# Kernel optimization log

Hardware: AMD Instinct MI355X
Metric: run time of the kernel (lower is better)

Reference implementation:

```python
import jax, jax.numpy as jnp
import numpy as np

GROUP = 8
BS = 4096
CH = 512


def setup_inputs() -> dict:
    key = jax.random.key(0)
    k1, k2 = jax.random.split(key)
    x = jax.random.normal(k1, (GROUP, BS, CH), dtype=jnp.float32)
    stdv = 1.0 / np.sqrt(CH)  # reset_parameters: uniform(-stdv, stdv), stdv = 1/sqrt(channels)
    weight = jax.random.uniform(k2, (GROUP, CH, CH), minval=-stdv, maxval=stdv, dtype=jnp.float32)
    return {"x": x, "weight": weight}


def reference(x, weight):
    """Sequential per-channel Householder reflections.

    x: (group, bs, channels); weight: (group, channels, channels).
    Step i uses v_i = weight[:, :, i] and applies
        x <- x - 2/(v^T v) * (x @ v) v^T
    """
    vs = jnp.transpose(weight, (2, 0, 1))  # (channels, group, channels): scan axis first

    def step(x, v):
        denom = jnp.sum(v * v, axis=-1)          # (group,)   v^T v
        proj = jnp.einsum('gbc,gc->gb', x, v)    # (group, bs) x @ v
        x = x - (2.0 / denom)[:, None, None] * proj[:, :, None] * v[:, None, :]
        return x, None

    x, _ = jax.lax.scan(step, x, vs)
    return x
```

## Files before the change

kernel.cpp:

```cpp
#include <hip/hip_runtime.h>

#define GROUP 8
#define BS 4096
#define CH 512
#define PW 32
#define NPANEL 16

typedef __attribute__((ext_vector_type(4))) float f32x4;
typedef __attribute__((ext_vector_type(8))) short bf16x8;
typedef __attribute__((ext_vector_type(8))) unsigned short u16x8;
typedef unsigned short u16;

static __device__ __forceinline__ u16 f2bf(float f) {
    unsigned int u = __builtin_bit_cast(unsigned int, f);
    u += 0x7FFFu + ((u >> 16) & 1u);
    return (u16)(u >> 16);
}
static __device__ __forceinline__ float bf2f(u16 h) {
    return __builtin_bit_cast(float, (unsigned int)h << 16);
}
static __device__ __forceinline__ void split8(const float* v, bf16x8& h, bf16x8& l) {
#pragma unroll
    for (int j = 0; j < 8; ++j) {
        u16 hu = f2bf(v[j]);
        h[j] = (short)hu;
        l[j] = (short)f2bf(v[j] - bf2f(hu));
    }
}
#define MFMA(a, b, c) __builtin_amdgcn_mfma_f32_16x16x32_bf16(a, b, c, 0, 0, 0)

typedef const __attribute__((address_space(1))) void* gas_t;
typedef __attribute__((address_space(3))) void* las_t;
static __device__ __forceinline__ void gload16(const void* g, void* l) {
    __builtin_amdgcn_global_load_lds((gas_t)g, (las_t)l, 16, 0, 0);
}


__global__ __launch_bounds__(1024) void k_panelprep(const float* __restrict__ w,
                                                    const float* __restrict__ x,
                                                    u16* __restrict__ Yfh,
                                                    u16* __restrict__ Yfl,
                                                    u16* __restrict__ Mfh,
                                                    u16* __restrict__ Mfl,
                                                    u16* __restrict__ Afh,
                                                    u16* __restrict__ Afl,
                                                    u16* __restrict__ xb) {
    __shared__ float Ylds[PW][516];
    __shared__ float Sp[16][PW][36];
    __shared__ float S_ls[PW][36];
    __shared__ float T_ls[PW][36];

    int bid = blockIdx.x;
    int t   = threadIdx.x;

    if (bid >= 128) {
        int bx  = bid - 128;
        int xcd = bx & 7;
        int j   = bx >> 3;
        const int UPG = (BS * CH) / 8;
        int base = xcd * UPG + j * (UPG / 128);
        for (int u = t; u < 2048; u += 1024) {
            int i = base + u;
            const float4* s = (const float4*)(x + (size_t)i * 8);
            float4 a = s[0], b = s[1];
            u16x8 o;
            o[0] = f2bf(a.x); o[1] = f2bf(a.y); o[2] = f2bf(a.z); o[3] = f2bf(a.w);
            o[4] = f2bf(b.x); o[5] = f2bf(b.y); o[6] = f2bf(b.z); o[7] = f2bf(b.w);
            *(u16x8*)(xb + (size_t)i * 8) = o;
        }
        return;
    }

    int pb   = (bid & 7) * 16 + (bid >> 3);
    int lane = t & 63;
    int wv   = t >> 6;
    int fr   = lane & 15;
    int kg   = lane >> 4;
    int g    = pb >> 4;
    int p    = pb & 15;
    int i0   = p * PW;

    const float* wg = w + (size_t)g * CH * CH;
    for (int idx4 = t; idx4 < 4096; idx4 += 1024) {
        int c = idx4 >> 3, f4 = idx4 & 7;
        float4 v = *(const float4*)(wg + (size_t)c * CH + i0 + f4 * 4);
        Ylds[f4 * 4 + 0][c] = v.x;
        Ylds[f4 * 4 + 1][c] = v.y;
        Ylds[f4 * 4 + 2][c] = v.z;
        Ylds[f4 * 4 + 3][c] = v.w;
    }
    __syncthreads();

    {
        f32x4 sacc[2][2];
#pragma unroll
        for (int a = 0; a < 2; ++a)
#pragma unroll
            for (int b = 0; b < 2; ++b)
#pragma unroll
                for (int z = 0; z < 4; ++z) sacc[a][b][z] = 0.f;
        {
            int kk = wv;
            bf16x8 fh[2], fl[2];
#pragma unroll
            for (int h = 0; h < 2; ++h) {
                float a8[8];
                const float* src = &Ylds[h * 16 + fr][kk * 32 + kg * 8];
#pragma unroll
                for (int j = 0; j < 8; ++j) a8[j] = src[j];
                split8(a8, fh[h], fl[h]);
            }
#pragma unroll
            for (int a = 0; a < 2; ++a)
#pragma unroll
                for (int b = 0; b < 2; ++b) {
                    sacc[a][b] = MFMA(fh[a], fh[b], sacc[a][b]);
                    sacc[a][b] = MFMA(fh[a], fl[b], sacc[a][b]);
                    sacc[a][b] = MFMA(fl[a], fh[b], sacc[a][b]);
                }
        }
#pragma unroll
        for (int a = 0; a < 2; ++a)
#pragma unroll
            for (int b = 0; b < 2; ++b)
#pragma unroll
                for (int j = 0; j < 4; ++j)
                    Sp[wv][a * 16 + kg * 4 + j][b * 16 + fr] = sacc[a][b][j];
    }
    __syncthreads();
    for (int idx = t; idx < PW * PW; idx += 1024) {
        int r = idx >> 5, c = idx & 31;
        float s = 0.f;
#pragma unroll
        for (int q = 0; q < 16; ++q) s += Sp[q][r][c];
        S_ls[r][c] = s;
    }
    __syncthreads();

    if (wv == 0) {
        float Trow[PW];
#pragma unroll
        for (int j = 0; j < PW; ++j) Trow[j] = 0.f;
        if (lane < PW) Trow[lane] = 2.0f / S_ls[lane][lane];
#pragma unroll
        for (int k = 1; k < PW; ++k) {
            float acc = 0.f;
#pragma unroll
            for (int j = 0; j < PW; ++j)
                if (j < k) acc += Trow[j] * S_ls[j][k];
            float bk = 2.0f / S_ls[k][k];
            if (lane < k) Trow[k] = -bk * acc;
        }
        if (lane < PW)
#pragma unroll
            for (int j = 0; j < PW; ++j) T_ls[lane][j] = Trow[j];
    }
    __syncthreads();

    u16* Msth = (u16*)Sp;
    u16* Mstl = Msth + 16384;
    {
        bf16x8 tbh[2], tbl[2];
#pragma unroll
        for (int cf = 0; cf < 2; ++cf) {
            float t8[8];
            const float* src = &T_ls[cf * 16 + fr][kg * 8];
#pragma unroll
            for (int j = 0; j < 8; ++j) t8[j] = src[j];
            split8(t8, tbh[cf], tbl[cf]);
        }
#pragma unroll
        for (int rfi = 0; rfi < 2; ++rfi) {
            int rf = 2 * wv + rfi;
            float a8[8];
#pragma unroll
            for (int j = 0; j < 8; ++j) a8[j] = Ylds[kg * 8 + j][rf * 16 + fr];
            bf16x8 ah, al;
            split8(a8, ah, al);
#pragma unroll
            for (int cf = 0; cf < 2; ++cf) {
                f32x4 m;
#pragma unroll
                for (int z = 0; z < 4; ++z) m[z] = 0.f;
                m = MFMA(ah, tbh[cf], m);
                m = MFMA(ah, tbl[cf], m);
                m = MFMA(al, tbh[cf], m);
#pragma unroll
                for (int j = 0; j < 4; ++j) {
                    int c  = rf * 16 + kg * 4 + j;
                    int ii = cf * 16 + fr;
                    int off = ((c >> 4)) * 512 + ((ii >> 3) * 16 + (c & 15)) * 8 + (ii & 7);
                    u16 hu = f2bf(m[j]);
                    Msth[off] = hu;
                    Mstl[off] = f2bf(m[j] - bf2f(hu));
                }
            }
        }
    }
    __syncthreads();
    {
        u16* Mfh_g = Mfh + (size_t)g * CH * CH + (size_t)p * 16384;
        u16* Mfl_g = Mfl + (size_t)g * CH * CH + (size_t)p * 16384;
        for (int idx = t; idx < 2048; idx += 1024) {
            *(bf16x8*)(Mfh_g + (size_t)idx * 8) = *(const bf16x8*)(Msth + idx * 8);
            *(bf16x8*)(Mfl_g + (size_t)idx * 8) = *(const bf16x8*)(Mstl + idx * 8);
        }
    }

    {
        u16* Yfh_g = Yfh + (size_t)g * CH * CH;
        u16* Yfl_g = Yfl + (size_t)g * CH * CH;
        for (int idx = t; idx < 32 * 64; idx += 1024) {
            int tile = idx >> 6, l2 = idx & 63;
            int itl = tile >> 4, ct = tile & 15;
            int row = l2 & 15, kgg = l2 >> 4;
            float a8[8];
            const float* src = &Ylds[itl * 16 + row][ct * 32 + kgg * 8];
#pragma unroll
            for (int j = 0; j < 8; ++j) a8[j] = src[j];
            bf16x8 h, l;
            split8(a8, h, l);
            size_t off = ((size_t)((2 * p + itl) * 16 + ct)) * 512 + (size_t)l2 * 8;
            *(bf16x8*)(Yfh_g + off) = h;
            *(bf16x8*)(Yfl_g + off) = l;
        }
    }

    {
        u16* Afh_g = Afh + (size_t)g * CH * CH;
        u16* Afl_g = Afl + (size_t)g * CH * CH;
        for (int idx = t; idx < 32 * 64; idx += 1024) {
            int mt = idx >> 6, l2 = idx & 63;
            int row = l2 & 15, kg2 = l2 >> 4;
            float a8[8];
#pragma unroll
            for (int j = 0; j < 8; ++j) a8[j] = Ylds[kg2 * 8 + j][mt * 16 + row];
            bf16x8 h, l;
            split8(a8, h, l);
            size_t off = ((size_t)(p * 32 + mt)) * 512 + (size_t)l2 * 8;
            *(bf16x8*)(Afh_g + off) = h;
            *(bf16x8*)(Afl_g + off) = l;
        }
    }
}

template<int W>
__global__ __launch_bounds__(512) void k_combine(const u16* __restrict__ Yfh,
                                                 const u16* __restrict__ Yfl,
                                                 u16* __restrict__ Mfh,
                                                 u16* __restrict__ Mfl) {
    constexpr int NF   = W / 16;
    constexpr int KSPL = (NF >= 8) ? 1 : 8 / NF;
    constexpr int CPW  = (NF + 7) / 8;

    __shared__ u16 MAh[16][520];
    __shared__ u16 MAl[16][520];
    __shared__ float Cl[16][W + 4];
    __shared__ float Cpart[(KSPL > 1) ? (KSPL - 1) : 1][16][W + 4];

    int bid = blockIdx.x;
    int cb  = (bid & 7) * 16 + (bid >> 3);
    int t = threadIdx.x, lane = t & 63, wv = t >> 6;
    int fr = lane & 15, kg = lane >> 4;
    int g  = cb >> 4;
    int sg = cb & 15;
    constexpr int SP = W / 16;
    int q  = sg / SP, rs = sg % SP;
    int i_top0 = 2 * q * W + rs * 16;
    int i_bot0 = 2 * q * W + W;

    const u16* Yfh_g = Yfh + (size_t)g * CH * CH;
    const u16* Yfl_g = Yfl + (size_t)g * CH * CH;
    u16* Mfh_g = Mfh + (size_t)g * CH * CH;
    u16* Mfl_g = Mfl + (size_t)g * CH * CH;

    int kt_top = i_top0 >> 5;
    int hh     = (i_top0 & 31) >> 3;

    for (int idx = t; idx < 1024; idx += 512) {
        int c = idx >> 1, sub = idx & 1;
        size_t off = ((size_t)(kt_top * 32 + (c >> 4))) * 512
                   + (size_t)((hh + sub) * 16 + (c & 15)) * 8;
        bf16x8 hv = *(const bf16x8*)(Mfh_g + off);
        bf16x8 lv = *(const bf16x8*)(Mfl_g + off);
#pragma unroll
        for (int j = 0; j < 8; ++j) {
            MAh[sub * 8 + j][c] = (u16)hv[j];
            MAl[sub * 8 + j][c] = (u16)lv[j];
        }
    }
    __syncthreads();

    int ibt = i_bot0 >> 4;

    if constexpr (KSPL == 1) {
        f32x4 accC[CPW];
#pragma unroll
        for (int nfi = 0; nfi < CPW; ++nfi)
#pragma unroll
            for (int z = 0; z < 4; ++z) accC[nfi][z] = 0.f;

        auto LOADY = [&](int ks, bf16x8* dh, bf16x8* dl) {
#pragma unroll
            for (int nfi = 0; nfi < CPW; ++nfi) {
                int nf = wv + 8 * nfi;
                size_t yo = ((size_t)((ibt + nf) * 16 + ks)) * 512 + (size_t)lane * 8;
                dh[nfi] = *(const bf16x8*)(Yfh_g + yo);
                dl[nfi] = *(const bf16x8*)(Yfl_g + yo);
            }
        };

        bf16x8 pbh[CPW], pbl[CPW];
        LOADY(0, pbh, pbl);
#pragma unroll
        for (int ks = 0; ks < 16; ++ks) {
            bf16x8 qbh[CPW], qbl[CPW];
            if (ks + 1 < 16) LOADY(ks + 1, qbh, qbl);
            bf16x8 ah = *(const bf16x8*)&MAh[fr][ks * 32 + kg * 8];
            bf16x8 al = *(const bf16x8*)&MAl[fr][ks * 32 + kg * 8];
#pragma unroll
            for (int nfi = 0; nfi < CPW; ++nfi) {
                accC[nfi] = MFMA(ah, pbh[nfi], accC[nfi]);
                accC[nfi] = MFMA(ah, pbl[nfi], accC[nfi]);
                accC[nfi] = MFMA(al, pbh[nfi], accC[nfi]);
            }
#pragma unroll
            for (int nfi = 0; nfi < CPW; ++nfi) { pbh[nfi] = qbh[nfi]; pbl[nfi] = qbl[nfi]; }
        }
#pragma unroll
        for (int nfi = 0; nfi < CPW; ++nfi) {
            int nf = wv + 8 * nfi;
#pragma unroll
            for (int jj = 0; jj < 4; ++jj)
                Cl[kg * 4 + jj][nf * 16 + fr] = accC[nfi][jj];
        }
        __syncthreads();
    } else {
        int nf  = wv % NF;
        int ksl = wv / NF;
        constexpr int KCH = 16 / KSPL;
        f32x4 accC;
#pragma unroll
        for (int z = 0; z < 4; ++z) accC[z] = 0.f;

        auto LOADY1 = [&](int ks, bf16x8& dh, bf16x8& dl) {
            size_t yo = ((size_t)((ibt + nf) * 16 + ks)) * 512 + (size_t)lane * 8;
            dh = *(const bf16x8*)(Yfh_g + yo);
            dl = *(const bf16x8*)(Yfl_g + yo);
        };

        bf16x8 pbh, pbl;
        LOADY1(ksl * KCH, pbh, pbl);
#pragma unroll
        for (int ki = 0; ki < KCH; ++ki) {
            int ks = ksl * KCH + ki;
            bf16x8 qbh, qbl;
            if (ki + 1 < KCH) LOADY1(ks + 1, qbh, qbl);
            bf16x8 ah = *(const bf16x8*)&MAh[fr][ks * 32 + kg * 8];
            bf16x8 al = *(const bf16x8*)&MAl[fr][ks * 32 + kg * 8];
            accC = MFMA(ah, pbh, accC);
            accC = MFMA(ah, pbl, accC);
            accC = MFMA(al, pbh, accC);
            pbh = qbh; pbl = qbl;
        }
        if (ksl == 0) {
#pragma unroll
            for (int jj = 0; jj < 4; ++jj)
                Cl[kg * 4 + jj][nf * 16 + fr] = accC[jj];
        } else {
#pragma unroll
            for (int jj = 0; jj < 4; ++jj)
                Cpart[ksl - 1][kg * 4 + jj][nf * 16 + fr] = accC[jj];
        }
        __syncthreads();
        for (int idx = t; idx < 16 * W; idx += 512) {
            int r = idx / W, c = idx - r * W;
            float s = Cl[r][c];
#pragma unroll
            for (int u = 0; u < KSPL - 1; ++u) s += Cpart[u][r][c];
            Cl[r][c] = s;
        }
        __syncthreads();
    }

    f32x4 accU[4];
#pragma unroll
    for (int ni = 0; ni < 4; ++ni)
#pragma unroll
        for (int z = 0; z < 4; ++z) accU[ni][z] = 0.f;

    int kt_bot = i_bot0 >> 5;
    constexpr int NKS2 = W / 32;

    auto LOADM = [&](int ks2, bf16x8* dh, bf16x8* dl) {
#pragma unroll
        for (int ni = 0; ni < 4; ++ni) {
            int ct = wv * 4 + ni;
            size_t mo = ((size_t)((kt_bot + ks2) * 32 + ct)) * 512 + (size_t)lane * 8;
            dh[ni] = *(const bf16x8*)(Mfh_g + mo);
            dl[ni] = *(const bf16x8*)(Mfl_g + mo);
        }
    };

    {
        bf16x8 mph[4], mpl[4];
        LOADM(0, mph, mpl);
#pragma unroll
        for (int ks2 = 0; ks2 < NKS2; ++ks2) {
            bf16x8 mqh[4], mql[4];
            if (ks2 + 1 < NKS2) LOADM(ks2 + 1, mqh, mql);
            float a8[8];
#pragma unroll
            for (int j = 0; j < 8; ++j) a8[j] = Cl[fr][ks2 * 32 + kg * 8 + j];
            bf16x8 ah2, al2;
            split8(a8, ah2, al2);
#pragma unroll
            for (int ni = 0; ni < 4; ++ni) {
                accU[ni] = MFMA(ah2, mph[ni], accU[ni]);
                accU[ni] = MFMA(ah2, mpl[ni], accU[ni]);
                accU[ni] = MFMA(al2, mph[ni], accU[ni]);
            }
#pragma unroll
            for (int ni = 0; ni < 4; ++ni) { mph[ni] = mqh[ni]; mpl[ni] = mql[ni]; }
        }
    }
#pragma unroll
    for (int ni = 0; ni < 4; ++ni) {
        int c = (wv * 4 + ni) * 16 + fr;
#pragma unroll
        for (int jj = 0; jj < 4; ++jj) {
            int il = kg * 4 + jj;
            float ma = bf2f(MAh[il][c]) + bf2f(MAl[il][c]);
            float m2 = ma - accU[ni][jj];
            u16 hu = f2bf(m2);
            MAh[il][c] = hu;
            MAl[il][c] = f2bf(m2 - bf2f(hu));
        }
    }
    __syncthreads();

    for (int idx = t; idx < 1024; idx += 512) {
        int c = idx >> 1, sub = idx & 1;
        bf16x8 hv, lv;
#pragma unroll
        for (int j = 0; j < 8; ++j) {
            hv[j] = (short)MAh[sub * 8 + j][c];
            lv[j] = (short)MAl[sub * 8 + j][c];
        }
        size_t off = ((size_t)(kt_top * 32 + (c >> 4))) * 512
                   + (size_t)((hh + sub) * 16 + (c & 15)) * 8;
        *(bf16x8*)(Mfh_g + off) = hv;
        *(bf16x8*)(Mfl_g + off) = lv;
    }
}

__global__ __launch_bounds__(256) void k_qbuild2(const u16* __restrict__ Afh,
                                                 const u16* __restrict__ Afl,
                                                 const u16* __restrict__ Mfh,
                                                 const u16* __restrict__ Mfl,
                                                 u16* __restrict__ Qt) {
    int bid = blockIdx.x;
    int qb  = (bid & 7) * 64 + (bid >> 3);
    int t = threadIdx.x, lane = t & 63, wv = t >> 6;
    int fr = lane & 15, kg = lane >> 4;
    int g  = qb >> 6;
    int tm = (qb >> 2) & 15, tn = qb & 3;
    int c0 = tm * 32;
    int d0 = tn * 128 + wv * 32;

    const u16* Afh_g = Afh + (size_t)g * CH * CH;
    const u16* Afl_g = Afl + (size_t)g * CH * CH;
    const u16* Mfh_g = Mfh + (size_t)g * CH * CH;
    const u16* Mfl_g = Mfl + (size_t)g * CH * CH;
    u16* Qt_g = Qt + (size_t)g * CH * CH;

    f32x4 acc[2][2];
#pragma unroll
    for (int mi = 0; mi < 2; ++mi)
#pragma unroll
        for (int ni = 0; ni < 2; ++ni)
#pragma unroll
            for (int z = 0; z < 4; ++z) acc[mi][ni][z] = 0.f;

    int mt0 = c0 >> 4;
    for (int ks = 0; ks < 16; ++ks) {
        bf16x8 ah[2], al[2], bh[2], bl[2];
#pragma unroll
        for (int mi = 0; mi < 2; ++mi) {
            size_t ao = ((size_t)(ks * 32 + mt0 + mi)) * 512 + (size_t)lane * 8;
            ah[mi] = *(const bf16x8*)(Afh_g + ao);
            al[mi] = *(const bf16x8*)(Afl_g + ao);
        }
#pragma unroll
        for (int ni = 0; ni < 2; ++ni) {
            int ct = (d0 >> 4) + ni;
            size_t mo = ((size_t)(ks * 32 + ct)) * 512 + (size_t)lane * 8;
            bh[ni] = *(const bf16x8*)(Mfh_g + mo);
            bl[ni] = *(const bf16x8*)(Mfl_g + mo);
        }
#pragma unroll
        for (int mi = 0; mi < 2; ++mi)
#pragma unroll
            for (int ni = 0; ni < 2; ++ni) {
                acc[mi][ni] = MFMA(ah[mi], bh[ni], acc[mi][ni]);
                acc[mi][ni] = MFMA(ah[mi], bl[ni], acc[mi][ni]);
                acc[mi][ni] = MFMA(al[mi], bh[ni], acc[mi][ni]);
            }
    }
#pragma unroll
    for (int mi = 0; mi < 2; ++mi)
#pragma unroll
        for (int ni = 0; ni < 2; ++ni) {
            int cb2 = c0 + mi * 16 + kg * 4;
            int d   = d0 + ni * 16 + fr;
            ushort4 h4;
            h4.x = f2bf(((cb2 + 0 == d) ? 1.0f : 0.0f) - acc[mi][ni][0]);
            h4.y = f2bf(((cb2 + 1 == d) ? 1.0f : 0.0f) - acc[mi][ni][1]);
            h4.z = f2bf(((cb2 + 2 == d) ? 1.0f : 0.0f) - acc[mi][ni][2]);
            h4.w = f2bf(((cb2 + 3 == d) ? 1.0f : 0.0f) - acc[mi][ni][3]);
            *(ushort4*)(Qt_g + (size_t)d * CH + cb2) = h4;
        }
}

__global__ __launch_bounds__(256) void k_gemm2(const u16* __restrict__ xb,
                                               const u16* __restrict__ Qt,
                                               float* __restrict__ out) {
    __shared__ u16 Ab[2][128 * 32];
    __shared__ u16 Bb[2][128 * 32];

    int bid0 = blockIdx.x;
    int wg = (bid0 & 7) * 128 + (bid0 >> 3);
    int g  = wg >> 7;
    int r  = wg & 127;
    int tm = r >> 2;
    int tn = r & 3;

    int t    = threadIdx.x;
    int lane = t & 63;
    int wv   = t >> 6;
    int wr   = wv >> 1, wc = wv & 1;
    int fr   = lane & 15, kg = lane >> 4;

    const u16* xg  = xb + (size_t)g * BS * CH + (size_t)tm * 128 * CH;
    const u16* Qtg = Qt + (size_t)g * CH * CH + (size_t)tn * 128 * CH;
    float* og = out + (size_t)g * BS * CH + (size_t)tm * 128 * CH + (size_t)tn * 128;

    f32x4 acc[4][4];
#pragma unroll
    for (int mi = 0; mi < 4; ++mi)
#pragma unroll
        for (int ni = 0; ni < 4; ++ni)
#pragma unroll
            for (int z = 0; z < 4; ++z) acc[mi][ni][z] = 0.f;

    int srow = lane >> 2;
    int scol = (lane & 3) * 8;

    auto STAGE = [&](int p, int ks) {
        int k0 = ks * 32;
#pragma unroll
        for (int si = 0; si < 2; ++si) {
            int seg = wv * 2 + si;
            int row = seg * 16 + srow;
            gload16(xg  + (size_t)row * CH + k0 + scol, &Ab[p][seg * 512]);
            gload16(Qtg + (size_t)row * CH + k0 + scol, &Bb[p][seg * 512]);
        }
    };

    STAGE(0, 0);
    asm volatile("s_waitcnt vmcnt(0)" ::: "memory");
    __builtin_amdgcn_s_barrier();

    for (int ks = 0; ks < 16; ++ks) {
        int cur = ks & 1;
        if (ks < 15) {
            STAGE(cur ^ 1, ks + 1);
            asm volatile("s_waitcnt vmcnt(4)" ::: "memory");
        } else {
            asm volatile("s_waitcnt vmcnt(0)" ::: "memory");
        }
        __builtin_amdgcn_s_barrier();

        bf16x8 af[4], bfr[4];
#pragma unroll
        for (int mi = 0; mi < 4; ++mi)
            af[mi] = *(const bf16x8*)&Ab[cur][(wr * 64 + mi * 16 + fr) * 32 + kg * 8];
#pragma unroll
        for (int ni = 0; ni < 4; ++ni)
            bfr[ni] = *(const bf16x8*)&Bb[cur][(wc * 64 + ni * 16 + fr) * 32 + kg * 8];
        __builtin_amdgcn_s_setprio(1);
#pragma unroll
        for (int mi = 0; mi < 4; ++mi)
#pragma unroll
            for (int ni = 0; ni < 4; ++ni)
                acc[mi][ni] = MFMA(af[mi], bfr[ni], acc[mi][ni]);
        __builtin_amdgcn_s_setprio(0);

        asm volatile("" ::: "memory");
        __builtin_amdgcn_s_barrier();
    }

    int rg = lane >> 4;
#pragma unroll
    for (int mi = 0; mi < 4; ++mi)
#pragma unroll
        for (int ni = 0; ni < 4; ++ni)
#pragma unroll
            for (int rj = 0; rj < 4; ++rj) {
                int grow = wr * 64 + mi * 16 + rg * 4 + rj;
                int gcol = wc * 64 + ni * 16 + fr;
                og[(size_t)grow * CH + gcol] = acc[mi][ni][rj];
            }
}

#define LDP 40
__global__ __launch_bounds__(256) void k_gemm_f32(const float* __restrict__ x,
                                                  const u16* __restrict__ Qt,
                                                  float* __restrict__ out) {
    __shared__ u16 Al[128 * LDP];
    __shared__ u16 Bl[128 * LDP];

    int bid = blockIdx.x;
    int g  = bid >> 7;
    int tn = (bid >> 5) & 3;
    int tm = bid & 31;

    int t    = threadIdx.x;
    int lane = t & 63;
    int w    = t >> 6;
    int wr   = w >> 1, wc = w & 1;

    const float* xg = x + (size_t)g * BS * CH + (size_t)tm * 128 * CH;
    const u16* Qtg = Qt + (size_t)g * CH * CH + (size_t)tn * 128 * CH;
    float* og = out + (size_t)g * BS * CH + (size_t)tm * 128 * CH + (size_t)tn * 128;

    f32x4 acc[4][4];
#pragma unroll
    for (int mi = 0; mi < 4; ++mi)
#pragma unroll
        for (int ni = 0; ni < 4; ++ni)
#pragma unroll
            for (int z = 0; z < 4; ++z) acc[mi][ni][z] = 0.f;

    int a_k4 = t & 7;
    int a_r  = t >> 3;
    int b_n  = t & 127;
    int b_kh = t >> 7;
    int fr = lane & 15, kg = lane >> 4;

    for (int ks = 0; ks < 16; ++ks) {
        int k0 = ks * 32;
        __syncthreads();
#pragma unroll
        for (int rr = 0; rr < 4; ++rr) {
            int r = a_r + 32 * rr;
            float4 v = *(const float4*)(xg + (size_t)r * CH + k0 + a_k4 * 4);
            ushort4 h;
            h.x = f2bf(v.x); h.y = f2bf(v.y); h.z = f2bf(v.z); h.w = f2bf(v.w);
            *(ushort4*)(&Al[r * LDP + a_k4 * 4]) = h;
        }
        {
            const u16* src = Qtg + (size_t)b_n * CH + k0 + b_kh * 16;
            u16x8 lo = *(const u16x8*)src;
            u16x8 hi = *(const u16x8*)(src + 8);
            *(u16x8*)(&Bl[b_n * LDP + b_kh * 16]) = lo;
            *(u16x8*)(&Bl[b_n * LDP + b_kh * 16 + 8]) = hi;
        }
        __syncthreads();
        bf16x8 af[4], bfr[4];
#pragma unroll
        for (int mi = 0; mi < 4; ++mi)
            af[mi] = *(const bf16x8*)(&Al[(wr * 64 + mi * 16 + fr) * LDP + kg * 8]);
#pragma unroll
        for (int ni = 0; ni < 4; ++ni)
            bfr[ni] = *(const bf16x8*)(&Bl[(wc * 64 + ni * 16 + fr) * LDP + kg * 8]);
#pragma unroll
        for (int mi = 0; mi < 4; ++mi)
#pragma unroll
            for (int ni = 0; ni < 4; ++ni)
                acc[mi][ni] = MFMA(af[mi], bfr[ni], acc[mi][ni]);
    }

    int rg = lane >> 4;
#pragma unroll
    for (int mi = 0; mi < 4; ++mi)
#pragma unroll
        for (int ni = 0; ni < 4; ++ni)
#pragma unroll
            for (int rj = 0; rj < 4; ++rj) {
                int grow = wr * 64 + mi * 16 + rg * 4 + rj;
                int gcol = wc * 64 + ni * 16 + fr;
                og[(size_t)grow * CH + gcol] = acc[mi][ni][rj];
            }
}

extern "C" void kernel_launch(void* const* d_in, const int* in_sizes, int n_in,
                              void* d_out, int out_size, void* d_ws, size_t ws_size,
                              hipStream_t stream) {
    const float* x = (const float*)d_in[0];
    const float* w = (const float*)d_in[1];
    float* out = (float*)d_out;

    char* ob = (char*)d_out;
    u16* Yfh = (u16*)ob;
    u16* Yfl = (u16*)(ob + (4u  << 20));
    u16* Mfh = (u16*)(ob + (8u  << 20));
    u16* Mfl = (u16*)(ob + (12u << 20));
    u16* Afh = (u16*)(ob + (16u << 20));
    u16* Afl = (u16*)(ob + (20u << 20));

    int fat = (ws_size >= ((32u << 20) + (4u << 20))) ? 1 : 0;
    u16* xbp = (u16*)d_ws;
    u16* Qt  = fat ? (u16*)((char*)d_ws + (32u << 20)) : (u16*)d_ws;

    k_panelprep<<<dim3(fat ? 1152 : 128), dim3(1024), 0, stream>>>(w, x, Yfh, Yfl, Mfh, Mfl, Afh, Afl, xbp);
    k_combine<32><<<dim3(128), dim3(512), 0, stream>>>(Yfh, Yfl, Mfh, Mfl);
    k_combine<64><<<dim3(128), dim3(512), 0, stream>>>(Yfh, Yfl, Mfh, Mfl);
    k_combine<128><<<dim3(128), dim3(512), 0, stream>>>(Yfh, Yfl, Mfh, Mfl);
    k_combine<256><<<dim3(128), dim3(512), 0, stream>>>(Yfh, Yfl, Mfh, Mfl);
    k_qbuild2<<<dim3(512), dim3(256), 0, stream>>>(Afh, Afl, Mfh, Mfl, Qt);
    if (fat)
        k_gemm2<<<dim3(1024), dim3(256), 0, stream>>>(xbp, Qt, out);
    else
        k_gemm_f32<<<dim3(1024), dim3(256), 0, stream>>>(x, Qt, out);
}
```

Measured before the change: 102.0 us.

## Spread x bf16 cast across combine and qbuild kernels to fill idle CUs

The fp32-to-bf16 cast of x used to run entirely as extra blocks of the panel-prep kernel. It is now split by group: three groups stay in panelprep, one group goes to each of the four combine launches, and one to qbuild2, each as extra blocks appended to that grid. The combine kernels launch only 128 blocks, so the extra cast blocks are meant to use otherwise idle CUs and hide the bandwidth-bound cast behind latency-bound stages. The cost is larger grids and more code in those kernels, and the cast blocks may compete for bandwidth with the main work.

```diff
diff --git a/kernel.cpp b/kernel.cpp
--- a/kernel.cpp
+++ b/kernel.cpp
@@ -34,6 +34,21 @@
 static __device__ __forceinline__ void gload16(const void* g, void* l) {
     __builtin_amdgcn_global_load_lds((gas_t)g, (las_t)l, 16, 0, 0);
 }
+
+static __device__ __forceinline__ void xcast_chunk(const float* __restrict__ x,
+                                                   u16* __restrict__ xb,
+                                                   int base, int t, int nthr) {
+    for (int u = t; u < 1024; u += nthr) {
+        int i = base + u;
+        const float4* s = (const float4*)(x + (size_t)i * 8);
+        float4 a = s[0], b = s[1];
+        u16x8 o;
+        o[0] = f2bf(a.x); o[1] = f2bf(a.y); o[2] = f2bf(a.z); o[3] = f2bf(a.w);
+        o[4] = f2bf(b.x); o[5] = f2bf(b.y); o[6] = f2bf(b.z); o[7] = f2bf(b.w);
+        *(u16x8*)(xb + (size_t)i * 8) = o;
+    }
+}
+#define UPG 262144
 
 
 __global__ __launch_bounds__(1024) void k_panelprep(const float* __restrict__ w,
@@ -54,20 +69,9 @@
     int t   = threadIdx.x;
 
     if (bid >= 128) {
-        int bx  = bid - 128;
-        int xcd = bx & 7;
-        int j   = bx >> 3;
-        const int UPG = (BS * CH) / 8;
-        int base = xcd * UPG + j * (UPG / 128);
-        for (int u = t; u < 2048; u += 1024) {
-            int i = base + u;
-            const float4* s = (const float4*)(x + (size_t)i * 8);
-            float4 a = s[0], b = s[1];
-            u16x8 o;
-            o[0] = f2bf(a.x); o[1] = f2bf(a.y); o[2] = f2bf(a.z); o[3] = f2bf(a.w);
-            o[4] = f2bf(b.x); o[5] = f2bf(b.y); o[6] = f2bf(b.z); o[7] = f2bf(b.w);
-            *(u16x8*)(xb + (size_t)i * 8) = o;
-        }
+        int b = bid - 128;
+        int gs = b >> 8, j = b & 255;
+        xcast_chunk(x, xb, gs * UPG + j * 1024, t, 1024);
         return;
     }
 
@@ -244,11 +248,13 @@
     }
 }
 
-template<int W>
+template<int W, int XG>
 __global__ __launch_bounds__(512) void k_combine(const u16* __restrict__ Yfh,
                                                  const u16* __restrict__ Yfl,
                                                  u16* __restrict__ Mfh,
-                                                 u16* __restrict__ Mfl) {
+                                                 u16* __restrict__ Mfl,
+                                                 const float* __restrict__ x,
+                                                 u16* __restrict__ xb) {
     constexpr int NF   = W / 16;
     constexpr int KSPL = (NF >= 8) ? 1 : 8 / NF;
     constexpr int CPW  = (NF + 7) / 8;
@@ -259,8 +265,15 @@
     __shared__ float Cpart[(KSPL > 1) ? (KSPL - 1) : 1][16][W + 4];
 
     int bid = blockIdx.x;
+    int t = threadIdx.x;
+
+    if (bid >= 128) {
+        xcast_chunk(x, xb, XG * UPG + (bid - 128) * 1024, t, 512);
+        return;
+    }
+
     int cb  = (bid & 7) * 16 + (bid >> 3);
-    int t = threadIdx.x, lane = t & 63, wv = t >> 6;
+    int lane = t & 63, wv = t >> 6;
     int fr = lane & 15, kg = lane >> 4;
     int g  = cb >> 4;
     int sg = cb & 15;
@@ -458,10 +471,19 @@
                                                  const u16* __restrict__ Afl,
                                                  const u16* __restrict__ Mfh,
                                                  const u16* __restrict__ Mfl,
-                                                 u16* __restrict__ Qt) {
+                                                 u16* __restrict__ Qt,
+                                                 const float* __restrict__ x,
+                                                 u16* __restrict__ xb) {
     int bid = blockIdx.x;
+    int t = threadIdx.x;
+
+    if (bid >= 512) {
+        xcast_chunk(x, xb, 7 * UPG + (bid - 512) * 1024, t, 256);
+        return;
+    }
+
     int qb  = (bid & 7) * 64 + (bid >> 3);
-    int t = threadIdx.x, lane = t & 63, wv = t >> 6;
+    int lane = t & 63, wv = t >> 6;
     int fr = lane & 15, kg = lane >> 4;
     int g  = qb >> 6;
     int tm = (qb >> 2) & 15, tn = qb & 3;
@@ -713,12 +735,12 @@
     u16* xbp = (u16*)d_ws;
     u16* Qt  = fat ? (u16*)((char*)d_ws + (32u << 20)) : (u16*)d_ws;
 
-    k_panelprep<<<dim3(fat ? 1152 : 128), dim3(1024), 0, stream>>>(w, x, Yfh, Yfl, Mfh, Mfl, Afh, Afl, xbp);
-    k_combine<32><<<dim3(128), dim3(512), 0, stream>>>(Yfh, Yfl, Mfh, Mfl);
-    k_combine<64><<<dim3(128), dim3(512), 0, stream>>>(Yfh, Yfl, Mfh, Mfl);
-    k_combine<128><<<dim3(128), dim3(512), 0, stream>>>(Yfh, Yfl, Mfh, Mfl);
-    k_combine<256><<<dim3(128), dim3(512), 0, stream>>>(Yfh, Yfl, Mfh, Mfl);
-    k_qbuild2<<<dim3(512), dim3(256), 0, stream>>>(Afh, Afl, Mfh, Mfl, Qt);
+    k_panelprep<<<dim3(fat ? 896 : 128), dim3(1024), 0, stream>>>(w, x, Yfh, Yfl, Mfh, Mfl, Afh, Afl, xbp);
+    k_combine<32, 3><<<dim3(fat ? 384 : 128), dim3(512), 0, stream>>>(Yfh, Yfl, Mfh, Mfl, x, xbp);
+    k_combine<64, 4><<<dim3(fat ? 384 : 128), dim3(512), 0, stream>>>(Yfh, Yfl, Mfh, Mfl, x, xbp);
+    k_combine<128, 5><<<dim3(fat ? 384 : 128), dim3(512), 0, stream>>>(Yfh, Yfl, Mfh, Mfl, x, xbp);
+    k_combine<256, 6><<<dim3(fat ? 384 : 128), dim3(512), 0, stream>>>(Yfh, Yfl, Mfh, Mfl, x, xbp);
+    k_qbuild2<<<dim3(fat ? 768 : 512), dim3(256), 0, stream>>>(Afh, Afl, Mfh, Mfl, Qt, x, xbp);
     if (fat)
         k_gemm2<<<dim3(1024), dim3(256), 0, stream>>>(xbp, Qt, out);
     else
```

Result: slower. 107.2 us (+5.1%).
